# Optimization experiments

Hardware: AMD Instinct MI355X
Metric: run time of the kernel (lower is better)

## Reference

```python
import jax, jax.numpy as jnp
import numpy as np

B, N, FIN, H, D = 4, 2048, 128, 4, 64
ALPHA = 0.2  # LeakyReLU negative slope


def _xavier_uniform(key, shape):
    fan_in, fan_out = shape[0], shape[1]
    limit = float(np.sqrt(6.0 / (fan_in + fan_out)))
    return jax.random.uniform(key, shape, jnp.float32, -limit, limit)


def setup_inputs() -> dict:
    key = jax.random.key(0)
    k1, k2, k3, k4 = jax.random.split(key, 4)
    x = jax.random.normal(k1, (B, N, FIN), jnp.float32)
    adj = jax.random.randint(k2, (B, N, N), 0, 2, jnp.int32)  # dense 0/1 mask
    W = _xavier_uniform(k3, (FIN, H * D))
    a = _xavier_uniform(k4, (2 * D, 1))
    return {"x": x, "adj": adj, "W": W, "a": a}


def reference(x, adj, W, a):
    Bb, Nn, _ = x.shape
    Dd = a.shape[0] // 2
    Hh = W.shape[1] // Dd
    # h: [B, N, H, D]
    h = (x @ W).reshape(Bb, Nn, Hh, Dd)
    # Additive attention: e[b,i,j,h] = leakyrelu(a1 . h[b,i,h] + a2 . h[b,j,h])
    a1 = a[:Dd, 0]
    a2 = a[Dd:, 0]
    ei = jnp.einsum('bnhd,d->bnh', h, a1)  # source (row i) term
    ej = jnp.einsum('bnhd,d->bnh', h, a2)  # dest (col j) term
    e = ei[:, :, None, :] + ej[:, None, :, :]  # [B, N, N, H]
    e = jnp.where(e >= 0, e, ALPHA * e)  # LeakyReLU
    e = jnp.where(adj[..., None] == 0, -jnp.inf, e)
    att = jax.nn.softmax(e, axis=2)  # softmax over neighbors j
    # dropout is a no-op in eval mode (training=False)
    out = jnp.einsum('bijh,bjhd->bihd', att, h)  # [B, N, H, D]
    return out.mean(axis=2)  # mean over heads -> [B, N, D]
```

## Files before the change

### kernel.cpp

```cpp
#include <hip/hip_runtime.h>

#define NN 2048
#define NH 4
#define DD 64
#define FIN 128
#define NB 4
#define LOG2E 1.44269504f

typedef unsigned short u16;
typedef unsigned int u32;
typedef short sh8 __attribute__((ext_vector_type(8)));
typedef float f32x4 __attribute__((ext_vector_type(4)));

static __device__ __forceinline__ u16 f2bf(float f) {
    u32 u = __builtin_bit_cast(u32, f);
    u += 0x7fffu + ((u >> 16) & 1u);
    return (u16)(u >> 16);
}
static __device__ __forceinline__ u32 pk_bf(float a, float b) {
    u32 ua = __builtin_bit_cast(u32, a) + 0x8000u;
    u32 ub = __builtin_bit_cast(u32, b) + 0x8000u;
    return __builtin_amdgcn_perm(ub, ua, 0x07060302u);
}
static __device__ __forceinline__ float fast_exp2(float x) {
    float r;
    asm("v_exp_f32 %0, %1" : "=v"(r) : "v"(x));
    return r;
}

static __device__ __forceinline__ void cd_probe(int ln15, int q, int* irow, int* icol) {
    sh8 pa, pb, qa, qb;
    #pragma unroll
    for (int ii = 0; ii < 8; ++ii) {
        pa[ii] = (short)f2bf((float)ln15);
        pb[ii] = 0;
        qa[ii] = 0;
        qb[ii] = (short)f2bf((float)ln15);
    }
    if (q == 0) { pb[0] = (short)f2bf(1.0f); qa[0] = (short)f2bf(1.0f); }
    f32x4 z = {};
    f32x4 prow = __builtin_amdgcn_mfma_f32_16x16x32_bf16(pa, pb, z, 0, 0, 0);
    f32x4 pcol = __builtin_amdgcn_mfma_f32_16x16x32_bf16(qa, qb, z, 0, 0, 0);
    #pragma unroll
    for (int r = 0; r < 4; ++r) {
        irow[r] = (int)(prow[r] + 0.5f);
        icol[r] = (int)(pcol[r] + 0.5f);
    }
}


__global__ __launch_bounds__(256)
void k_pack(const int* __restrict__ adj, const float* __restrict__ W,
            u32* __restrict__ msk, u16* __restrict__ WT) {
    const int tid = threadIdx.x;
    if (blockIdx.x < 2048) {
        const int wid  = (blockIdx.x * 256 + tid) >> 6;
        const int lane = tid & 63;
        for (int t = wid; t < NB * NN * 8; t += 8192) {
            const int c256 = t & 7;
            const int i    = (t >> 3) & (NN - 1);
            const int b    = t >> 14;
            const int4 v = *(const int4*)(adj + ((size_t)(b * NN + i)) * NN + c256 * 256 + lane * 4);
            u32 nib = (v.x ? 1u : 0u) | (v.y ? 2u : 0u) | (v.z ? 4u : 0u) | (v.w ? 8u : 0u);
            u32 w = nib << (4 * (lane & 7));
            w |= __shfl_xor(w, 1);
            w |= __shfl_xor(w, 2);
            w |= __shfl_xor(w, 4);
            if ((lane & 7) == 0)
                msk[((size_t)(b * 64 + c256 * 8 + (lane >> 3))) * NN + i] = w;
        }
    } else {
        const int bt  = blockIdx.x - 2048;
        const int kt  = bt & 3;
        const int ct8 = bt >> 2;
        __shared__ float tile[32][33];
        const int rr = tid >> 5, cc = tid & 31;
        #pragma unroll
        for (int i = 0; i < 4; ++i)
            tile[rr + 8 * i][cc] = W[(size_t)(kt * 32 + rr + 8 * i) * 256 + ct8 * 32 + cc];
        __syncthreads();
        #pragma unroll
        for (int i = 0; i < 4; ++i)
            WT[(size_t)(ct8 * 32 + rr + 8 * i) * FIN + kt * 32 + cc] = f2bf(tile[cc][rr + 8 * i]);
    }
}

__global__ __launch_bounds__(256)
void k_gemm_h(const float* __restrict__ x, const u16* __restrict__ WT,
              const float* __restrict__ a,
              u16* __restrict__ hTf, float* __restrict__ ei_g, float* __restrict__ ej_g) {
    const int nb = blockIdx.x, b = blockIdx.y;
    const int tid = threadIdx.x, hd = tid >> 6, lane = tid & 63, ln15 = lane & 15, q = lane >> 4;
    const int q8 = q * 8;
    const int n0 = nb * 64;

    __shared__ u16 xs[64][136];
    __shared__ float cs[NH][4][16][20];
    {
        const int col = (tid & 31) * 4;
        const int r0  = tid >> 5;
        #pragma unroll
        for (int rr = 0; rr < 8; ++rr) {
            const int row = r0 + rr * 8;
            const float4 v = *(const float4*)(x + ((size_t)(b * NN + n0 + row)) * FIN + col);
            *(u32*)&xs[row][col]     = pk_bf(v.x, v.y);
            *(u32*)&xs[row][col + 2] = pk_bf(v.z, v.w);
        }
    }
    __syncthreads();

    int irow[4], icol[4];
    cd_probe(ln15, q, irow, icol);

    f32x4 acc[4][4] = {};
    #pragma unroll
    for (int ks = 0; ks < 4; ++ks) {
        sh8 af[4], bfr[4];
        #pragma unroll
        for (int ct = 0; ct < 4; ++ct)
            af[ct] = *(const sh8*)(WT + (size_t)(hd * 64 + ct * 16 + ln15) * FIN + ks * 32 + q8);
        #pragma unroll
        for (int nt = 0; nt < 4; ++nt)
            bfr[nt] = *(const sh8*)&xs[nt * 16 + ln15][ks * 32 + q8];
        #pragma unroll
        for (int ct = 0; ct < 4; ++ct)
            #pragma unroll
            for (int nt = 0; nt < 4; ++nt)
                acc[ct][nt] = __builtin_amdgcn_mfma_f32_16x16x32_bf16(af[ct], bfr[nt], acc[ct][nt], 0, 0, 0);
    }

    float eip[4] = {}, ejq[4] = {};
    #pragma unroll
    for (int ct = 0; ct < 4; ++ct) {
        #pragma unroll
        for (int nt = 0; nt < 4; ++nt)
            #pragma unroll
            for (int r = 0; r < 4; ++r)
                cs[hd][nt][irow[r]][icol[r]] = acc[ct][nt][r];

        #pragma unroll
        for (int p = 0; p < 2; ++p) {
            const float4 c0 = *(const float4*)&cs[hd][2 * p + (q >> 1)][ln15][(q & 1) * 8];
            const float4 c1 = *(const float4*)&cs[hd][2 * p + (q >> 1)][ln15][(q & 1) * 8 + 4];
            uint4 o;
            o.x = pk_bf(c0.x, c0.y); o.y = pk_bf(c0.z, c0.w);
            o.z = pk_bf(c1.x, c1.y); o.w = pk_bf(c1.z, c1.w);
            *(uint4*)(hTf + ((((size_t)(b * NH + hd) * 64 + nb * 2 + p) * 4 + ct) * 512) + lane * 8) = o;
        }

        float a1v[4], a2v[4];
        #pragma unroll
        for (int r = 0; r < 4; ++r) {
            const int d = ct * 16 + 4 * q + r;
            a1v[r] = a[d] * LOG2E;
            a2v[r] = a[64 + d] * LOG2E;
        }
        #pragma unroll
        for (int nt = 0; nt < 4; ++nt)
            #pragma unroll
            for (int r = 0; r < 4; ++r) {
                const float v = cs[hd][nt][4 * q + r][ln15];
                eip[nt] += v * a1v[r];
                ejq[nt] += v * a2v[r];
            }
    }
    #pragma unroll
    for (int nt = 0; nt < 4; ++nt) {
        eip[nt] += __shfl_xor(eip[nt], 16);
        eip[nt] += __shfl_xor(eip[nt], 32);
        ejq[nt] += __shfl_xor(ejq[nt], 16);
        ejq[nt] += __shfl_xor(ejq[nt], 32);
    }
    if (lane < 16) {
        const size_t bhd = (size_t)(b * NH + hd) * NN;
        #pragma unroll
        for (int nt = 0; nt < 4; ++nt) {
            ei_g[bhd + n0 + nt * 16 + lane] = eip[nt];
            ej_g[bhd + n0 + nt * 16 + lane] = ejq[nt];
        }
    }
}

__global__ __launch_bounds__(256, 3)
void k_attn(const u32* __restrict__ msk, const u16* __restrict__ hTf,
            const float* __restrict__ ei_g, const float* __restrict__ ej_g,
            float* __restrict__ o_part, float* __restrict__ l_part, int nj) {
    const int ib = blockIdx.x, js = blockIdx.y, b = blockIdx.z;
    const int js_n = gridDim.y;
    const int tid = threadIdx.x, hd = tid >> 6, lane = tid & 63, ln15 = lane & 15, q = lane >> 4;
    const int q8 = q * 8;
    const int iA = ib * 32 + ln15;

    int irow[4], icol[4];
    cd_probe(ln15, q, irow, icol);

    const size_t bhd = (size_t)(b * NH + hd) * NN;
    const float eivA = ei_g[bhd + iA];
    const float eivB = ei_g[bhd + iA + 16];
    const u32*   mptr = msk + (size_t)(b * 64) * NN;
    const float* ejp  = ej_g + bhd + q8;
    const u16*   hfp  = hTf + (size_t)(b * NH + hd) * (64 * 2048) + (size_t)lane * 8;

    sh8 ones;
    #pragma unroll
    for (int ii = 0; ii < 8; ++ii) ones[ii] = (short)0x3F80;

    f32x4 acc[8] = {};
    f32x4 accl[2] = {};

    const int jt0 = js * nj;
    u32 mA = mptr[(size_t)jt0 * NN + iA];
    u32 mB = mptr[(size_t)jt0 * NN + iA + 16];
    float4 e0 = *(const float4*)(ejp + jt0 * 32);
    float4 e1 = *(const float4*)(ejp + jt0 * 32 + 4);
    sh8 h0 = *(const sh8*)(hfp + (size_t)jt0 * 2048);
    sh8 h1 = *(const sh8*)(hfp + (size_t)jt0 * 2048 + 512);
    sh8 h2 = *(const sh8*)(hfp + (size_t)jt0 * 2048 + 1024);
    sh8 h3 = *(const sh8*)(hfp + (size_t)jt0 * 2048 + 1536);

    for (int t = 0; t < nj; ++t) {
        const int tn = (t + 1 < nj) ? jt0 + t + 1 : jt0;
        const u32 mAn = mptr[(size_t)tn * NN + iA];
        const u32 mBn = mptr[(size_t)tn * NN + iA + 16];
        const float4 e0n = *(const float4*)(ejp + tn * 32);
        const float4 e1n = *(const float4*)(ejp + tn * 32 + 4);
        const sh8 h0n = *(const sh8*)(hfp + (size_t)tn * 2048);
        const sh8 h1n = *(const sh8*)(hfp + (size_t)tn * 2048 + 512);
        const sh8 h2n = *(const sh8*)(hfp + (size_t)tn * 2048 + 1024);
        const sh8 h3n = *(const sh8*)(hfp + (size_t)tn * 2048 + 1536);

        const float ef[8] = { e0.x, e0.y, e0.z, e0.w, e1.x, e1.y, e1.z, e1.w };
        const u32 mqA = mA >> q8;
        const u32 mqB = mB >> q8;
        float pA[8], pB[8];
        #pragma unroll
        for (int ii = 0; ii < 8; ++ii) {
            float eA = eivA + ef[ii];
            float eB = eivB + ef[ii];
            eA = fmaxf(eA, 0.2f * eA);
            eB = fmaxf(eB, 0.2f * eB);
            const float xA = fast_exp2(eA);
            const float xB = fast_exp2(eB);
            pA[ii] = (mqA & (1u << ii)) ? xA : 0.f;
            pB[ii] = (mqB & (1u << ii)) ? xB : 0.f;
        }
        union { uint4 u; sh8 v; } avA, avB;
        avA.u.x = pk_bf(pA[0], pA[1]); avA.u.y = pk_bf(pA[2], pA[3]);
        avA.u.z = pk_bf(pA[4], pA[5]); avA.u.w = pk_bf(pA[6], pA[7]);
        avB.u.x = pk_bf(pB[0], pB[1]); avB.u.y = pk_bf(pB[2], pB[3]);
        avB.u.z = pk_bf(pB[4], pB[5]); avB.u.w = pk_bf(pB[6], pB[7]);

        acc[0] = __builtin_amdgcn_mfma_f32_16x16x32_bf16(avA.v, h0, acc[0], 0, 0, 0);
        acc[1] = __builtin_amdgcn_mfma_f32_16x16x32_bf16(avA.v, h1, acc[1], 0, 0, 0);
        acc[2] = __builtin_amdgcn_mfma_f32_16x16x32_bf16(avA.v, h2, acc[2], 0, 0, 0);
        acc[3] = __builtin_amdgcn_mfma_f32_16x16x32_bf16(avA.v, h3, acc[3], 0, 0, 0);
        accl[0] = __builtin_amdgcn_mfma_f32_16x16x32_bf16(avA.v, ones, accl[0], 0, 0, 0);
        acc[4] = __builtin_amdgcn_mfma_f32_16x16x32_bf16(avB.v, h0, acc[4], 0, 0, 0);
        acc[5] = __builtin_amdgcn_mfma_f32_16x16x32_bf16(avB.v, h1, acc[5], 0, 0, 0);
        acc[6] = __builtin_amdgcn_mfma_f32_16x16x32_bf16(avB.v, h2, acc[6], 0, 0, 0);
        acc[7] = __builtin_amdgcn_mfma_f32_16x16x32_bf16(avB.v, h3, acc[7], 0, 0, 0);
        accl[1] = __builtin_amdgcn_mfma_f32_16x16x32_bf16(avB.v, ones, accl[1], 0, 0, 0);

        mA = mAn; mB = mBn; e0 = e0n; e1 = e1n;
        h0 = h0n; h1 = h1n; h2 = h2n; h3 = h3n;
    }

    const size_t pbA = (((size_t)b * 128 + ib * 2 + 0) * js_n + js) * NH + hd;
    const size_t pbB = (((size_t)b * 128 + ib * 2 + 1) * js_n + js) * NH + hd;
    #pragma unroll
    for (int r = 0; r < 4; ++r) {
        l_part[pbA * 16 + irow[r]] = accl[0][r];
        l_part[pbB * 16 + irow[r]] = accl[1][r];
    }
    float* opA = o_part + pbA * 1024;
    float* opB = o_part + pbB * 1024;
    #pragma unroll
    for (int dt = 0; dt < 4; ++dt)
        #pragma unroll
        for (int r = 0; r < 4; ++r) {
            opA[(size_t)irow[r] * 64 + dt * 16 + icol[r]] = acc[dt][r];
            opB[(size_t)irow[r] * 64 + dt * 16 + icol[r]] = acc[4 + dt][r];
        }
}

template <int JS>
__global__ __launch_bounds__(256)
void k_combine(const float* __restrict__ o_part, const float* __restrict__ l_part,
               float* __restrict__ out) {
    const int ib = blockIdx.x, b = blockIdx.y;
    const int tid = threadIdx.x;
    const int i = tid >> 4, d4 = (tid & 15) * 4;
    float  lv[NH][JS];
    float4 ov[NH][JS];
    #pragma unroll
    for (int h = 0; h < NH; ++h)
        #pragma unroll
        for (int js = 0; js < JS; ++js) {
            const size_t pbase = (((size_t)b * 128 + ib) * JS + js) * NH + h;
            lv[h][js] = l_part[pbase * 16 + i];
            ov[h][js] = *(const float4*)(o_part + pbase * 1024 + (size_t)i * 64 + d4);
        }
    float4 sacc = {0.f, 0.f, 0.f, 0.f};
    #pragma unroll
    for (int h = 0; h < NH; ++h) {
        float l = 0.f;
        float4 oh = {0.f, 0.f, 0.f, 0.f};
        #pragma unroll
        for (int js = 0; js < JS; ++js) {
            l += lv[h][js];
            oh.x += ov[h][js].x; oh.y += ov[h][js].y;
            oh.z += ov[h][js].z; oh.w += ov[h][js].w;
        }
        const float inv = 0.25f / l;
        sacc.x += oh.x * inv; sacc.y += oh.y * inv;
        sacc.z += oh.z * inv; sacc.w += oh.w * inv;
    }
    *(float4*)(out + ((size_t)(b * NN) + ib * 16 + i) * DD + d4) = sacc;
}

extern "C" void kernel_launch(void* const* d_in, const int* in_sizes, int n_in,
                              void* d_out, int out_size, void* d_ws, size_t ws_size,
                              hipStream_t stream) {
    const float* x = nullptr; const int* adj = nullptr;
    const float* W = nullptr; const float* a = nullptr;
    for (int i = 0; i < n_in; ++i) {
        switch (in_sizes[i]) {
            case NB * NN * FIN:  x   = (const float*)d_in[i]; break;
            case NB * NN * NN:   adj = (const int*)d_in[i];   break;
            case FIN * 256:      W   = (const float*)d_in[i]; break;
            case 2 * DD:         a   = (const float*)d_in[i]; break;
            default: break;
        }
    }
    if (!x)   x   = (const float*)d_in[0];
    if (!adj) adj = (const int*)d_in[1];
    if (!W)   W   = (const float*)d_in[2];
    if (!a)   a   = (const float*)d_in[3];
    float* out = (float*)d_out;

    char* ws = (char*)d_ws;
    u16*   WT  = (u16*)(ws);
    float* ei  = (float*)(ws + 65536);
    float* ej  = (float*)(ws + 196608);
    u16*   hTf = (u16*)(ws + 327680);
    u32*   msk = (u32*)(ws + 4521984);
    float* l_p = (float*)(ws + 6619136);
    float* o_p = (float*)(ws + 7143424);

    const size_t need4 = 7143424 + (size_t)4 * 8388608;
    const size_t need2 = 7143424 + (size_t)2 * 8388608;
    const int js_n = (ws_size >= need4) ? 4 : (ws_size >= need2) ? 2 : 1;

    k_pack<<<dim3(2080), dim3(256), 0, stream>>>(adj, W, msk, WT);
    k_gemm_h<<<dim3(32, NB), dim3(256), 0, stream>>>(x, WT, a, hTf, ei, ej);
    k_attn<<<dim3(64, js_n, NB), dim3(256), 0, stream>>>(msk, hTf, ei, ej, o_p, l_p, 64 / js_n);
    if (js_n == 4)      k_combine<4><<<dim3(128, NB), dim3(256), 0, stream>>>(o_p, l_p, out);
    else if (js_n == 2) k_combine<2><<<dim3(128, NB), dim3(256), 0, stream>>>(o_p, l_p, out);
    else                k_combine<1><<<dim3(128, NB), dim3(256), 0, stream>>>(o_p, l_p, out);
}
```

Measured before the change: 144.2 us.

## Fuse adjacency bitmask packing into attention kernel via shared memory

Removes the separate adj-packing pass and its global bitmask round-trip. Each attention block now reads its own 32-row slab of the int32 adjacency directly, packs it into bits in shared memory, and reads the mask from LDS inside the loop. The tile count becomes a template parameter. This saves writing and re-reading the packed mask and one large launch. In exchange, the adjacency load moves into the attention kernel's prologue, which adds latency there before compute starts and uses extra LDS.

```diff
diff --git a/kernel.cpp b/kernel.cpp
--- a/kernel.cpp
+++ b/kernel.cpp
@@ -50,39 +50,20 @@
 
 
 __global__ __launch_bounds__(256)
-void k_pack(const int* __restrict__ adj, const float* __restrict__ W,
-            u32* __restrict__ msk, u16* __restrict__ WT) {
+void k_prep(const float* __restrict__ W, u16* __restrict__ WT) {
+    const int bt  = blockIdx.x;
+    const int kt  = bt & 3;
+    const int ct8 = bt >> 2;
+    __shared__ float tile[32][33];
     const int tid = threadIdx.x;
-    if (blockIdx.x < 2048) {
-        const int wid  = (blockIdx.x * 256 + tid) >> 6;
-        const int lane = tid & 63;
-        for (int t = wid; t < NB * NN * 8; t += 8192) {
-            const int c256 = t & 7;
-            const int i    = (t >> 3) & (NN - 1);
-            const int b    = t >> 14;
-            const int4 v = *(const int4*)(adj + ((size_t)(b * NN + i)) * NN + c256 * 256 + lane * 4);
-            u32 nib = (v.x ? 1u : 0u) | (v.y ? 2u : 0u) | (v.z ? 4u : 0u) | (v.w ? 8u : 0u);
-            u32 w = nib << (4 * (lane & 7));
-            w |= __shfl_xor(w, 1);
-            w |= __shfl_xor(w, 2);
-            w |= __shfl_xor(w, 4);
-            if ((lane & 7) == 0)
-                msk[((size_t)(b * 64 + c256 * 8 + (lane >> 3))) * NN + i] = w;
-        }
-    } else {
-        const int bt  = blockIdx.x - 2048;
-        const int kt  = bt & 3;
-        const int ct8 = bt >> 2;
-        __shared__ float tile[32][33];
-        const int rr = tid >> 5, cc = tid & 31;
-        #pragma unroll
-        for (int i = 0; i < 4; ++i)
-            tile[rr + 8 * i][cc] = W[(size_t)(kt * 32 + rr + 8 * i) * 256 + ct8 * 32 + cc];
-        __syncthreads();
-        #pragma unroll
-        for (int i = 0; i < 4; ++i)
-            WT[(size_t)(ct8 * 32 + rr + 8 * i) * FIN + kt * 32 + cc] = f2bf(tile[cc][rr + 8 * i]);
-    }
+    const int rr = tid >> 5, cc = tid & 31;
+    #pragma unroll
+    for (int i = 0; i < 4; ++i)
+        tile[rr + 8 * i][cc] = W[(size_t)(kt * 32 + rr + 8 * i) * 256 + ct8 * 32 + cc];
+    __syncthreads();
+    #pragma unroll
+    for (int i = 0; i < 4; ++i)
+        WT[(size_t)(ct8 * 32 + rr + 8 * i) * FIN + kt * 32 + cc] = f2bf(tile[cc][rr + 8 * i]);
 }
 
 __global__ __launch_bounds__(256)
@@ -181,15 +162,42 @@
     }
 }
 
+template <int NJT>
 __global__ __launch_bounds__(256, 3)
-void k_attn(const u32* __restrict__ msk, const u16* __restrict__ hTf,
+void k_attn(const int* __restrict__ adj, const u16* __restrict__ hTf,
             const float* __restrict__ ei_g, const float* __restrict__ ej_g,
-            float* __restrict__ o_part, float* __restrict__ l_part, int nj) {
+            float* __restrict__ o_part, float* __restrict__ l_part) {
     const int ib = blockIdx.x, js = blockIdx.y, b = blockIdx.z;
     const int js_n = gridDim.y;
     const int tid = threadIdx.x, hd = tid >> 6, lane = tid & 63, ln15 = lane & 15, q = lane >> 4;
     const int q8 = q * 8;
     const int iA = ib * 32 + ln15;
+    const int jt0 = js * NJT;
+
+    __shared__ u32 mlds[32][65];
+
+    {
+        const int row = (hd << 3) + (lane >> 3);
+        const int* abase = adj + (size_t)(b * NN + ib * 32 + row) * NN + jt0 * 32 + (lane & 7) * 4;
+        #pragma unroll
+        for (int jb = 0; jb < NJT; jb += 8) {
+            int4 vv[8];
+            #pragma unroll
+            for (int u = 0; u < 8; ++u)
+                vv[u] = *(const int4*)(abase + (jb + u) * 32);
+            #pragma unroll
+            for (int u = 0; u < 8; ++u) {
+                u32 nib = (vv[u].x ? 1u : 0u) | (vv[u].y ? 2u : 0u) |
+                          (vv[u].z ? 4u : 0u) | (vv[u].w ? 8u : 0u);
+                u32 w = nib << (4 * (lane & 7));
+                w |= __shfl_xor(w, 1);
+                w |= __shfl_xor(w, 2);
+                w |= __shfl_xor(w, 4);
+                if ((lane & 7) == 0) mlds[row][jb + u] = w;
+            }
+        }
+    }
+    __syncthreads();
 
     int irow[4], icol[4];
     cd_probe(ln15, q, irow, icol);
@@ -197,7 +205,6 @@
     const size_t bhd = (size_t)(b * NH + hd) * NN;
     const float eivA = ei_g[bhd + iA];
     const float eivB = ei_g[bhd + iA + 16];
-    const u32*   mptr = msk + (size_t)(b * 64) * NN;
     const float* ejp  = ej_g + bhd + q8;
     const u16*   hfp  = hTf + (size_t)(b * NH + hd) * (64 * 2048) + (size_t)lane * 8;
 
@@ -208,9 +215,8 @@
     f32x4 acc[8] = {};
     f32x4 accl[2] = {};
 
-    const int jt0 = js * nj;
-    u32 mA = mptr[(size_t)jt0 * NN + iA];
-    u32 mB = mptr[(size_t)jt0 * NN + iA + 16];
+    u32 mA = mlds[ln15][0];
+    u32 mB = mlds[ln15 + 16][0];
     float4 e0 = *(const float4*)(ejp + jt0 * 32);
     float4 e1 = *(const float4*)(ejp + jt0 * 32 + 4);
     sh8 h0 = *(const sh8*)(hfp + (size_t)jt0 * 2048);
@@ -218,10 +224,11 @@
     sh8 h2 = *(const sh8*)(hfp + (size_t)jt0 * 2048 + 1024);
     sh8 h3 = *(const sh8*)(hfp + (size_t)jt0 * 2048 + 1536);
 
-    for (int t = 0; t < nj; ++t) {
-        const int tn = (t + 1 < nj) ? jt0 + t + 1 : jt0;
-        const u32 mAn = mptr[(size_t)tn * NN + iA];
-        const u32 mBn = mptr[(size_t)tn * NN + iA + 16];
+    for (int t = 0; t < NJT; ++t) {
+        const int tn = (t + 1 < NJT) ? jt0 + t + 1 : jt0;
+        const int tl = (t + 1 < NJT) ? t + 1 : 0;
+        const u32 mAn = mlds[ln15][tl];
+        const u32 mBn = mlds[ln15 + 16][tl];
         const float4 e0n = *(const float4*)(ejp + tn * 32);
         const float4 e1n = *(const float4*)(ejp + tn * 32 + 4);
         const sh8 h0n = *(const sh8*)(hfp + (size_t)tn * 2048);
@@ -343,7 +350,6 @@
     float* ei  = (float*)(ws + 65536);
     float* ej  = (float*)(ws + 196608);
     u16*   hTf = (u16*)(ws + 327680);
-    u32*   msk = (u32*)(ws + 4521984);
     float* l_p = (float*)(ws + 6619136);
     float* o_p = (float*)(ws + 7143424);
 
@@ -351,9 +357,14 @@
     const size_t need2 = 7143424 + (size_t)2 * 8388608;
     const int js_n = (ws_size >= need4) ? 4 : (ws_size >= need2) ? 2 : 1;
 
-    k_pack<<<dim3(2080), dim3(256), 0, stream>>>(adj, W, msk, WT);
+    k_prep<<<dim3(32), dim3(256), 0, stream>>>(W, WT);
     k_gemm_h<<<dim3(32, NB), dim3(256), 0, stream>>>(x, WT, a, hTf, ei, ej);
-    k_attn<<<dim3(64, js_n, NB), dim3(256), 0, stream>>>(msk, hTf, ei, ej, o_p, l_p, 64 / js_n);
+    if (js_n == 4)
+        k_attn<16><<<dim3(64, 4, NB), dim3(256), 0, stream>>>(adj, hTf, ei, ej, o_p, l_p);
+    else if (js_n == 2)
+        k_attn<32><<<dim3(64, 2, NB), dim3(256), 0, stream>>>(adj, hTf, ei, ej, o_p, l_p);
+    else
+        k_attn<64><<<dim3(64, 1, NB), dim3(256), 0, stream>>>(adj, hTf, ei, ej, o_p, l_p);
     if (js_n == 4)      k_combine<4><<<dim3(128, NB), dim3(256), 0, stream>>>(o_p, l_p, out);
     else if (js_n == 2) k_combine<2><<<dim3(128, NB), dim3(256), 0, stream>>>(o_p, l_p, out);
     else                k_combine<1><<<dim3(128, NB), dim3(256), 0, stream>>>(o_p, l_p, out);
```

Result: faster. 138.2 us (-4.2%).
